# Performance work log

Measured on AMD Instinct MI355X. Metric: run time of the kernel, lower is better.

The kernel has to match this reference:

```python
import jax, jax.numpy as jnp
import numpy as np
from jax import lax

B, S = 2, 1024
T = B * S
HIDDEN, Q_LORA_RANK = 7168, 1536
N_HEADS, HEAD_DIM, ROPE_DIM = 64, 128, 64
INDEX_TOPK = 2048
QUANT_BLOCK = 128
F8_MAX = 448.0  # float8_e4m3fn max
SOFTMAX_SCALE = HEAD_DIM ** -0.5


def quant_dequant_ue8m0(x):
    """Simulate per-128-block fp8(e4m3) quantization with ue8m0 (power-of-2, ceil) scales."""
    shp = x.shape
    xb = x.reshape(shp[:-1] + (shp[-1] // QUANT_BLOCK, QUANT_BLOCK))
    amax = jnp.max(jnp.abs(xb), axis=-1, keepdims=True)
    scale = jnp.exp2(jnp.ceil(jnp.log2(jnp.maximum(amax, 1e-4) / F8_MAX)))
    q = jnp.clip(xb / scale, -F8_MAX, F8_MAX).astype(jnp.float8_e4m3fn).astype(jnp.float32)
    return (q * scale).reshape(shp)


def rope_cos_sin(positions):
    half = ROPE_DIM // 2
    inv_freq = 1.0 / (10000.0 ** (jnp.arange(half, dtype=jnp.float32) * 2.0 / ROPE_DIM))
    ang = positions.astype(jnp.float32)[:, None] * inv_freq[None, :]  # [T, half]
    return jnp.cos(ang), jnp.sin(ang)


def apply_rope(x, cos, sin):
    half = x.shape[-1] // 2
    x1, x2 = x[..., :half], x[..., half:]
    return jnp.concatenate([x1 * cos - x2 * sin, x1 * sin + x2 * cos], axis=-1)


def setup_inputs() -> dict:
    key = jax.random.key(0)
    k0, k1, k2, k3, k4 = jax.random.split(key, 5)
    std = 0.02
    hidden_states = jax.random.normal(k0, (T, HIDDEN), jnp.float32)
    q_lora = jax.random.normal(k1, (T, Q_LORA_RANK), jnp.float32)
    wq_b = jax.random.normal(k2, (N_HEADS * HEAD_DIM, Q_LORA_RANK), jnp.float32) * std
    wk = jax.random.normal(k3, (HEAD_DIM, HIDDEN), jnp.float32) * std
    k_norm_w = jnp.ones((HEAD_DIM,), jnp.float32)
    k_norm_b = jnp.zeros((HEAD_DIM,), jnp.float32)
    w_proj = jax.random.normal(k4, (N_HEADS, HIDDEN), jnp.float32) * std
    positions = jnp.tile(jnp.arange(S, dtype=jnp.int32), B)  # local position within each sequence
    seq_lens = jnp.full((B,), S, dtype=jnp.int32)
    return {"hidden_states": hidden_states, "q_lora": q_lora, "wq_b": wq_b, "wk": wk,
            "k_norm_w": k_norm_w, "k_norm_b": k_norm_b, "w_proj": w_proj,
            "positions": positions, "seq_lens": seq_lens}


def reference(hidden_states, q_lora, wq_b, wk, k_norm_w, k_norm_b, w_proj, positions, seq_lens):
    # --- projections ---
    q = (q_lora @ wq_b.T).reshape(T, N_HEADS, HEAD_DIM)
    k = hidden_states @ wk.T  # [T, HEAD_DIM]
    # k_norm: LayerNorm(head_dim, eps=1e-6) in fp32
    mu = jnp.mean(k, axis=-1, keepdims=True)
    kc = k - mu
    k = kc * lax.rsqrt(jnp.mean(kc * kc, axis=-1, keepdims=True) + 1e-6) * k_norm_w + k_norm_b
    # --- RoPE on first ROPE_DIM dims of q (per head) and k ---
    cos, sin = rope_cos_sin(positions)
    q = jnp.concatenate([apply_rope(q[..., :ROPE_DIM], cos[:, None, :], sin[:, None, :]),
                         q[..., ROPE_DIM:]], axis=-1)
    k = jnp.concatenate([apply_rope(k[..., :ROPE_DIM], cos, sin), k[..., ROPE_DIM:]], axis=-1)
    # --- fp8 ue8m0 quant-dequant (simulates q_fp8 / per_token_quant_and_transform) ---
    q = quant_dequant_ue8m0(q)
    k = quant_dequant_ue8m0(k)
    # --- head weights (weights_proj, head-count and softmax scaling folded in) ---
    weights = (hidden_states @ w_proj.T) * (N_HEADS ** -0.5) * SOFTMAX_SCALE  # [T, H]
    # --- variable-length causal bounds (compute_cu_seqlen_kv_bounds_nocache) ---
    cu = jnp.concatenate([jnp.zeros((1,), jnp.int32), jnp.cumsum(seq_lens).astype(jnp.int32)])
    batch_ids = jnp.repeat(jnp.arange(seq_lens.shape[0], dtype=jnp.int32), seq_lens,
                           total_repeat_length=T)
    ks_ = cu[batch_ids]                                   # start of each token's KV window
    local_pos = jnp.arange(T, dtype=jnp.int32) - ks_
    ke_ = ks_ + local_pos + 1                             # exclusive end (causal)
    pos_n = jnp.arange(T, dtype=jnp.int32)
    mask = (pos_n[None, :] >= ks_[:, None]) & (pos_n[None, :] < ke_[:, None])  # [T, T]
    # --- fp8_mqa_logits: logits[m,n] = sum_h w[m,h] * relu(q[m,h] . k[n]) ---
    qh = jnp.transpose(q, (1, 0, 2))  # [H, T, D]
    wh = weights.T                    # [H, T]
    def step(acc, hw):
        qh_i, w_i = hw
        return acc + jax.nn.relu(qh_i @ k.T) * w_i[:, None], None
    logits, _ = lax.scan(step, jnp.zeros((T, T), jnp.float32), (qh, wh))
    logits = jnp.where(mask, logits, -jnp.inf)
    # --- top-k selection + local-index remap ---
    k_take = min(INDEX_TOPK, T)
    _, idx = lax.top_k(logits, k_take)
    local = idx - ks_[:, None]
    valid = (local >= 0) & (idx < ke_[:, None])
    topk_indices = jnp.where(valid, local, -1).astype(jnp.int32)
    return logits, topk_indices
```

## Files before the change

kernel.cpp:

```cpp
#include <hip/hip_runtime.h>
#include <math.h>
#include <stdint.h>

#define T_TOK 2048
#define HIDDEN 7168
#define RANK 1536
#define NH 64
#define HD 128
#define NQ (NH*HD)
#define RH 32
#define KSPLIT 8
#define KCHUNK (HIDDEN/KSPLIT)
#define NKW 192

#define MASK_VAL (-3.0e38f)

typedef short bf16x8 __attribute__((ext_vector_type(8)));
typedef float f32x4  __attribute__((ext_vector_type(4)));

#define GLL16(src, dst) __builtin_amdgcn_global_load_lds( \
    (const __attribute__((address_space(1))) void*)(src), \
    (__attribute__((address_space(3))) void*)(dst), 16, 0, 0)

__device__ __forceinline__ float qd_e4m3(float x){
  float ax = fabsf(x);
  float s = (x < 0.f) ? -1.f : 1.f;
  float q;
  if (ax < 0.015625f) {
    q = rintf(ax * 512.f) * 0.001953125f;
  } else {
    int e; (void)frexpf(ax, &e);
    float quant = ldexpf(1.f, e - 4);
    q = rintf(ax / quant) * quant;
  }
  return s * q;
}

__device__ __forceinline__ float ue8m0_scale(float amax){
  float y = fmaxf(amax, 1e-4f) / 448.f;
  int e; float m = frexpf(y, &e);
  int ce = (m == 0.5f) ? (e - 1) : e;
  return ldexpf(1.f, ce);
}

__device__ __forceinline__ unsigned short f2bf_rne(float x){
  unsigned int u = __float_as_uint(x);
  unsigned int r = u + 0x7FFFu + ((u >> 16) & 1u);
  return (unsigned short)(r >> 16);
}

__device__ __forceinline__ void split_bf16(float x, unsigned short& hi, unsigned short& lo){
  unsigned int u = __float_as_uint(x);
  hi = (unsigned short)(u >> 16);
  float xh = __uint_as_float(u & 0xFFFF0000u);
  lo = f2bf_rne(x - xh);
}

__global__ void kt_cossin(const int* __restrict__ pos, float* __restrict__ cost,
                          float* __restrict__ sint){
  int idx = blockIdx.x*256 + threadIdx.x;
  if (idx >= T_TOK*RH) return;
  int t = idx >> 5, j = idx & 31;
  float ex = (float)(2*j) / 64.0f;
  float p10 = (float)pow(10000.0, (double)ex);
  float invf = 1.0f / p10;
  float ang = (float)pos[t] * invf;
  cost[idx] = (float)cos((double)ang);
  sint[idx] = (float)sin((double)ang);
}

__global__ __launch_bounds__(256) void kw_split(const float* __restrict__ Wk,
                                                const float* __restrict__ Wp,
                                                unsigned short* __restrict__ Bh,
                                                unsigned short* __restrict__ Bl){
  int idx = blockIdx.x*256 + threadIdx.x;
  int e0 = idx*8;
  if (e0 >= NKW*HIDDEN) return;
  int n = e0 / HIDDEN, k = e0 - n*HIDDEN;
  const float* src = (n < HD) ? (Wk + (size_t)n*HIDDEN + k) : (Wp + (size_t)(n-HD)*HIDDEN + k);
  float4 a0 = *(const float4*)src;
  float4 a1 = *(const float4*)(src+4);
  float f[8] = {a0.x,a0.y,a0.z,a0.w,a1.x,a1.y,a1.z,a1.w};
  unsigned short h[8], l[8];
  #pragma unroll
  for (int i=0;i<8;i++) split_bf16(f[i], h[i], l[i]);
  *(uint4*)(Bh + e0) = *(const uint4*)h;
  *(uint4*)(Bl + e0) = *(const uint4*)l;
}

__global__ __launch_bounds__(256,2) void kfat(const float* __restrict__ A,
                                              const float* __restrict__ B,
                                              const float* __restrict__ cost,
                                              const float* __restrict__ sint,
                                              unsigned short* __restrict__ q16,
                                              const float* __restrict__ H,
                                              const unsigned short* __restrict__ Bhg,
                                              const unsigned short* __restrict__ Blg,
                                              float* __restrict__ P){
  __shared__ char smem[33792] __attribute__((aligned(16)));
  int bid = blockIdx.x;
  int tid = threadIdx.x, lane = tid & 63;

  if (bid >= 256){
    int kb_id = bid - 256;
    unsigned short* Ah = (unsigned short*)smem;
    unsigned short* Al = Ah + 128*32;
    unsigned short* Bh = Al + 128*32;
    unsigned short* Bl = Bh + 128*32;
    float (*amx)[2] = (float(*)[2])(smem + 32768);
    int n0 = (kb_id & 63)*128, m0 = (kb_id >> 6)*128;
    int w = tid >> 6, wr = w >> 1, wc = w & 1;
    int row = tid >> 1, half = tid & 1;
    const float* Arow = A + (size_t)(m0+row)*RANK + half*16;
    const float* Brow = B + (size_t)(n0+row)*RANK + half*16;
    int sw = ((row >> 1) & 3) << 4;
    int wb0 = row*64 + half*32;
    f32x4 acc[4][4];
    #pragma unroll
    for (int i=0;i<4;i++)
      #pragma unroll
      for (int j=0;j<4;j++)
        #pragma unroll
        for (int r=0;r<4;r++) acc[i][j][r] = 0.f;

    for (int kb = 0; kb < RANK; kb += 32){
      float4 av4[4], bv4[4];
      #pragma unroll
      for (int c=0;c<4;c++) av4[c] = *(const float4*)(Arow + kb + 4*c);
      #pragma unroll
      for (int c=0;c<4;c++) bv4[c] = *(const float4*)(Brow + kb + 4*c);
      __syncthreads();
      {
        unsigned short h[16], l[16];
        const float* f = (const float*)av4;
        #pragma unroll
        for (int i=0;i<16;i++) split_bf16(f[i], h[i], l[i]);
        *(uint4*)((char*)Ah + ((wb0   )^sw)) = *(const uint4*)&h[0];
        *(uint4*)((char*)Ah + ((wb0+16)^sw)) = *(const uint4*)&h[8];
        *(uint4*)((char*)Al + ((wb0   )^sw)) = *(const uint4*)&l[0];
        *(uint4*)((char*)Al + ((wb0+16)^sw)) = *(const uint4*)&l[8];
        const float* g = (const float*)bv4;
        #pragma unroll
        for (int i=0;i<16;i++) split_bf16(g[i], h[i], l[i]);
        *(uint4*)((char*)Bh + ((wb0   )^sw)) = *(const uint4*)&h[0];
        *(uint4*)((char*)Bh + ((wb0+16)^sw)) = *(const uint4*)&h[8];
        *(uint4*)((char*)Bl + ((wb0   )^sw)) = *(const uint4*)&l[0];
        *(uint4*)((char*)Bl + ((wb0+16)^sw)) = *(const uint4*)&l[8];
      }
      __syncthreads();
      bf16x8 ah[4], bh[4], tmp[4];
      #pragma unroll
      for (int mf=0;mf<4;mf++){
        int rl = wr*64 + mf*16 + (lane&15);
        int ad = (rl*64 + ((lane>>4)*16)) ^ ((((rl>>1)&3))<<4);
        ah[mf] = *(const bf16x8*)((const char*)Ah + ad);
      }
      #pragma unroll
      for (int nf=0;nf<4;nf++){
        int rl = wc*64 + nf*16 + (lane&15);
        int ad = (rl*64 + ((lane>>4)*16)) ^ ((((rl>>1)&3))<<4);
        bh[nf] = *(const bf16x8*)((const char*)Bh + ad);
      }
      #pragma unroll
      for (int mf=0;mf<4;mf++)
        #pragma unroll
        for (int nf=0;nf<4;nf++)
          acc[mf][nf] = __builtin_amdgcn_mfma_f32_16x16x32_bf16(ah[mf], bh[nf], acc[mf][nf], 0,0,0);
      #pragma unroll
      for (int mf=0;mf<4;mf++){
        int rl = wr*64 + mf*16 + (lane&15);
        int ad = (rl*64 + ((lane>>4)*16)) ^ ((((rl>>1)&3))<<4);
        tmp[mf] = *(const bf16x8*)((const char*)Al + ad);
      }
      #pragma unroll
      for (int mf=0;mf<4;mf++)
        #pragma unroll
        for (int nf=0;nf<4;nf++)
          acc[mf][nf] = __builtin_amdgcn_mfma_f32_16x16x32_bf16(tmp[mf], bh[nf], acc[mf][nf], 0,0,0);
      #pragma unroll
      for (int nf=0;nf<4;nf++){
        int rl = wc*64 + nf*16 + (lane&15);
        int ad = (rl*64 + ((lane>>4)*16)) ^ ((((rl>>1)&3))<<4);
        tmp[nf] = *(const bf16x8*)((const char*)Bl + ad);
      }
      #pragma unroll
      for (int mf=0;mf<4;mf++)
        #pragma unroll
        for (int nf=0;nf<4;nf++)
          acc[mf][nf] = __builtin_amdgcn_mfma_f32_16x16x32_bf16(ah[mf], tmp[nf], acc[mf][nf], 0,0,0);
    }

    if (wc == 0){
      #pragma unroll
      for (int mf=0;mf<4;mf++)
        #pragma unroll
        for (int r=0;r<4;r++){
          int t = m0 + wr*64 + mf*16 + (lane>>4)*4 + r;
          #pragma unroll
          for (int nf=0;nf<2;nf++){
            int d0 = nf*16 + (lane&15);
            float c = cost[t*RH + d0], s = sint[t*RH + d0];
            float x1 = acc[mf][nf][r], x2 = acc[mf][nf+2][r];
            acc[mf][nf][r]   = __fsub_rn(__fmul_rn(x1,c), __fmul_rn(x2,s));
            acc[mf][nf+2][r] = __fadd_rn(__fmul_rn(x1,s), __fmul_rn(x2,c));
          }
        }
    }
    float pm[16];
    #pragma unroll
    for (int mf=0;mf<4;mf++)
      #pragma unroll
      for (int r=0;r<4;r++){
        float m1 = fmaxf(fabsf(acc[mf][0][r]), fabsf(acc[mf][1][r]));
        float m2 = fmaxf(fabsf(acc[mf][2][r]), fabsf(acc[mf][3][r]));
        pm[mf*4+r] = fmaxf(m1, m2);
      }
    #pragma unroll
    for (int msk=1; msk<16; msk<<=1)
      #pragma unroll
      for (int i=0;i<16;i++) pm[i] = fmaxf(pm[i], __shfl_xor(pm[i], msk, 16));
    if ((lane & 15) == 0){
      #pragma unroll
      for (int mf=0;mf<4;mf++)
        #pragma unroll
        for (int r=0;r<4;r++)
          amx[wr*64 + mf*16 + (lane>>4)*4 + r][wc] = pm[mf*4+r];
    }
    __syncthreads();
    #pragma unroll
    for (int mf=0;mf<4;mf++)
      #pragma unroll
      for (int r=0;r<4;r++){
        int rl = wr*64 + mf*16 + (lane>>4)*4 + r;
        int t = m0 + rl;
        float scl = ue8m0_scale(fmaxf(amx[rl][0], amx[rl][1]));
        #pragma unroll
        for (int nf=0;nf<4;nf++){
          float v = acc[mf][nf][r];
          float qv = qd_e4m3(v / scl) * scl;
          q16[(size_t)t*NQ + n0 + wc*64 + nf*16 + (lane&15)] = f2bf_rne(qv);
        }
      }
  } else {
    unsigned short* Ah = (unsigned short*)smem;
    unsigned short* Al = Ah + 64*32;
    unsigned short* Bh = Al + 64*32;
    unsigned short* Bl = Bh + NKW*32;
    int b2 = bid;
    int ks = b2 & 7, m0 = (b2 >> 3)*64, k0 = ks*KCHUNK;
    int w = tid >> 6, wr = w >> 1, wc = w & 1;
    int ar = tid >> 2, ac = (tid & 3)*8;
    const float* Arow = H + (size_t)(m0+ar)*HIDDEN + k0 + ac;
    int awb = (ar*64 + ac*2) ^ (((ar>>1)&3)<<4);
    f32x4 acc[2][6];
    #pragma unroll
    for (int i=0;i<2;i++)
      #pragma unroll
      for (int j=0;j<6;j++)
        #pragma unroll
        for (int r=0;r<4;r++) acc[i][j][r] = 0.f;

    for (int kb = 0; kb < KCHUNK; kb += 32){
      float4 a0 = *(const float4*)(Arow + kb);
      float4 a1 = *(const float4*)(Arow + kb + 4);
      __syncthreads();
      {
        float f[8] = {a0.x,a0.y,a0.z,a0.w,a1.x,a1.y,a1.z,a1.w};
        unsigned short h[8], l[8];
        #pragma unroll
        for (int i=0;i<8;i++) split_bf16(f[i], h[i], l[i]);
        *(uint4*)((char*)Ah + awb) = *(const uint4*)h;
        *(uint4*)((char*)Al + awb) = *(const uint4*)l;
      }
      #pragma unroll
      for (int i=0;i<3;i++){
        int ch = w + 4*i;
        int o = ch*1024 + lane*16;
        int row = o >> 6;
        int cb = (o & 63) ^ (((row>>1)&3)<<4);
        size_t srcoff = (size_t)row*HIDDEN + k0 + kb + (cb>>1);
        GLL16(Bhg + srcoff, (char*)Bh + ch*1024);
        GLL16(Blg + srcoff, (char*)Bl + ch*1024);
      }
      __syncthreads();
      bf16x8 ah[2], alr[2], bh[6], bl[6];
      #pragma unroll
      for (int mf=0;mf<2;mf++){
        int rl = wr*32 + mf*16 + (lane&15);
        int ad = (rl*64 + ((lane>>4)*16)) ^ (((rl>>1)&3)<<4);
        ah[mf]  = *(const bf16x8*)((const char*)Ah + ad);
        alr[mf] = *(const bf16x8*)((const char*)Al + ad);
      }
      #pragma unroll
      for (int nf=0;nf<6;nf++){
        int jl = wc*96 + nf*16 + (lane&15);
        int ad = (jl*64 + ((lane>>4)*16)) ^ (((jl>>1)&3)<<4);
        bh[nf] = *(const bf16x8*)((const char*)Bh + ad);
        bl[nf] = *(const bf16x8*)((const char*)Bl + ad);
      }
      #pragma unroll
      for (int mf=0;mf<2;mf++)
        #pragma unroll
        for (int nf=0;nf<6;nf++){
          acc[mf][nf] = __builtin_amdgcn_mfma_f32_16x16x32_bf16(ah[mf],  bh[nf], acc[mf][nf], 0,0,0);
          acc[mf][nf] = __builtin_amdgcn_mfma_f32_16x16x32_bf16(alr[mf], bh[nf], acc[mf][nf], 0,0,0);
          acc[mf][nf] = __builtin_amdgcn_mfma_f32_16x16x32_bf16(ah[mf],  bl[nf], acc[mf][nf], 0,0,0);
        }
    }
    #pragma unroll
    for (int mf=0;mf<2;mf++)
      #pragma unroll
      for (int r=0;r<4;r++){
        int t = m0 + wr*32 + mf*16 + (lane>>4)*4 + r;
        #pragma unroll
        for (int nf=0;nf<6;nf++){
          int n = wc*96 + nf*16 + (lane&15);
          P[((size_t)ks*T_TOK + t)*NKW + n] = acc[mf][nf][r];
        }
      }
  }
}

__global__ __launch_bounds__(128) void kc2(const float* __restrict__ P,
                                           const float* __restrict__ knw,
                                           const float* __restrict__ knb,
                                           const float* __restrict__ cost,
                                           const float* __restrict__ sint,
                                           unsigned short* __restrict__ k16,
                                           float* __restrict__ abuf){
  __shared__ float sh[128];
  __shared__ float red[128];
  int t = blockIdx.x, d = threadIdx.x;
  float v = 0.f;
  #pragma unroll
  for (int s=0;s<KSPLIT;s++) v += P[((size_t)s*T_TOK + t)*NKW + d];
  if (d < NH){
    float wv = 0.f;
    #pragma unroll
    for (int s=0;s<KSPLIT;s++) wv += P[((size_t)s*T_TOK + t)*NKW + HD + d];
    wv = wv * 0.125f;
    wv = wv * 0.08838834764831845f;
    abuf[(size_t)t*NH + d] = wv;
  }
  red[d] = v; __syncthreads();
  for (int s=64;s>0;s>>=1){ if (d<s) red[d] += red[d+s]; __syncthreads(); }
  float mu = red[0] * (1.0f/128.0f); __syncthreads();
  float kc = v - mu;
  red[d] = kc*kc; __syncthreads();
  for (int s=64;s>0;s>>=1){ if (d<s) red[d] += red[d+s]; __syncthreads(); }
  float var = red[0] * (1.0f/128.0f); __syncthreads();
  float rs = 1.0f / sqrtf(var + 1e-6f);
  float nv = ((kc * rs) * knw[d]) + knb[d];
  sh[d] = nv; __syncthreads();
  float rv;
  if (d < RH)            rv = sh[d]*cost[t*RH + d]      - sh[d+RH]*sint[t*RH + d];
  else if (d < 2*RH)     rv = sh[d-RH]*sint[t*RH + d-RH] + sh[d]*cost[t*RH + d-RH];
  else                   rv = nv;
  red[d] = fabsf(rv); __syncthreads();
  for (int s=64;s>0;s>>=1){ if (d<s) red[d] = fmaxf(red[d], red[d+s]); __syncthreads(); }
  float scale = ue8m0_scale(red[0]);
  k16[(size_t)t*HD + d] = f2bf_rne(qd_e4m3(rv / scale) * scale);
}

__global__ __launch_bounds__(256,2) void ke2(const unsigned short* __restrict__ q16,
                                             const unsigned short* __restrict__ k16,
                                             const float* __restrict__ W,
                                             const int* __restrict__ seq,
                                             float* __restrict__ out){
  __shared__ unsigned short Kt[128*128];
  __shared__ unsigned short Qt[2][64*128];
  __shared__ float Wl[64*64];
  int j0 = blockIdx.x*128, t0 = blockIdx.y*64;
  int tid = threadIdx.x;
  int s0 = seq[0];
  int ks0 = (t0 < s0) ? 0 : s0;
  if (j0 > t0 + 63 || j0 + 127 < ks0){
    int tl = tid >> 2, c0 = (tid & 3) * 32;
    float4 m4 = make_float4(MASK_VAL, MASK_VAL, MASK_VAL, MASK_VAL);
    float* rowp = out + (size_t)(t0+tl)*T_TOK + j0 + c0;
    #pragma unroll
    for (int c=0;c<32;c+=4) *(float4*)(rowp + c) = m4;
    return;
  }
  int lane = tid & 63, w = tid >> 6, wt = w >> 1, wj = w & 1;
  #pragma unroll
  for (int is=0; is<8; ++is){
    int o = is*4096 + w*1024 + lane*16;
    int row = o >> 8;
    int os = o ^ ((row & 7) << 4);
    int col = (os & 255) >> 1;
    GLL16(k16 + (size_t)(j0 + row)*HD + col, (char*)Kt + is*4096 + w*1024);
  }
  {
    int tl = tid >> 2, h0 = (tid & 3) * 16;
    float wv[16];
    #pragma unroll
    for (int c=0;c<4;c++) *(float4*)&wv[4*c] = *(const float4*)(W + (size_t)(t0+tl)*NH + h0 + 4*c);
    #pragma unroll
    for (int i=0;i<16;i++) Wl[(h0+i)*64 + tl] = wv[i];
  }
  #pragma unroll
  for (int is=0; is<4; ++is){
    int o = is*4096 + w*1024 + lane*16;
    int row = o >> 8;
    int os = o ^ ((row & 7) << 4);
    int col = (os & 255) >> 1;
    GLL16(q16 + (size_t)(t0 + row)*NQ + 0*HD + col, (char*)&Qt[0][0] + is*4096 + w*1024);
  }
  __syncthreads();
  bf16x8 bk[4][4];
  #pragma unroll
  for (int jf=0;jf<4;jf++){
    int jl = wj*64 + jf*16 + (lane&15);
    int sz = (jl & 7) << 4;
    #pragma unroll
    for (int kf=0;kf<4;kf++)
      bk[jf][kf] = *(const bf16x8*)((const char*)Kt + ((jl*256 + kf*64 + ((lane>>4)*16)) ^ sz));
  }
  bool skip = (j0 + wj*64 > t0 + wt*32 + 31) || (j0 + wj*64 + 63 < ks0);
  f32x4 acc[2][4];
  #pragma unroll
  for (int a=0;a<2;a++)
    #pragma unroll
    for (int b=0;b<4;b++)
      #pragma unroll
      for (int r=0;r<4;r++) acc[a][b][r] = 0.f;

  for (int h = 0; h < NH; ++h){
    if (h < NH-1){
      char* dst = (char*)&Qt[(h+1)&1][0];
      #pragma unroll
      for (int is=0; is<4; ++is){
        int o = is*4096 + w*1024 + lane*16;
        int row = o >> 8;
        int os = o ^ ((row & 7) << 4);
        int col = (os & 255) >> 1;
        GLL16(q16 + (size_t)(t0 + row)*NQ + (size_t)(h+1)*HD + col, dst + is*4096 + w*1024);
      }
    }
    if (!skip){
      const char* qb = (const char*)&Qt[h&1][0];
      bf16x8 aq[2][4];
      #pragma unroll
      for (int tf=0;tf<2;tf++){
        int tl = wt*32 + tf*16 + (lane&15);
        int sz = (tl & 7) << 4;
        #pragma unroll
        for (int kf=0;kf<4;kf++)
          aq[tf][kf] = *(const bf16x8*)(qb + ((tl*256 + kf*64 + ((lane>>4)*16)) ^ sz));
      }
      f32x4 pp[2][4];
      #pragma unroll
      for (int a=0;a<2;a++)
        #pragma unroll
        for (int b=0;b<4;b++)
          #pragma unroll
          for (int r=0;r<4;r++) pp[a][b][r] = 0.f;
      #pragma unroll
      for (int kf=0;kf<4;kf++)
        #pragma unroll
        for (int tf=0;tf<2;tf++)
          #pragma unroll
          for (int jf=0;jf<4;jf++)
            pp[tf][jf] = __builtin_amdgcn_mfma_f32_16x16x32_bf16(aq[tf][kf], bk[jf][kf], pp[tf][jf], 0,0,0);
      #pragma unroll
      for (int tf=0;tf<2;tf++)
        #pragma unroll
        for (int r=0;r<4;r++){
          float wv = Wl[h*64 + wt*32 + tf*16 + (lane>>4)*4 + r];
          #pragma unroll
          for (int jf=0;jf<4;jf++)
            acc[tf][jf][r] = fmaf(wv, fmaxf(pp[tf][jf][r], 0.f), acc[tf][jf][r]);
        }
    }
    __syncthreads();
  }
  #pragma unroll
  for (int tf=0;tf<2;tf++)
    #pragma unroll
    for (int r=0;r<4;r++){
      int t = t0 + wt*32 + tf*16 + (lane>>4)*4 + r;
      #pragma unroll
      for (int jf=0;jf<4;jf++){
        int j = j0 + wj*64 + jf*16 + (lane&15);
        bool ok = (j >= ks0) && (j <= t);
        out[(size_t)t*T_TOK + j] = ok ? acc[tf][jf][r] : MASK_VAL;
      }
    }
}

__global__ __launch_bounds__(256) void kf_topk(const float* __restrict__ logits,
                                               const int* __restrict__ seq,
                                               float* __restrict__ outIdx){
  __shared__ unsigned long long keys[1024];
  int t = blockIdx.x, tid = threadIdx.x;
  int s0 = seq[0];
  int ks = (t < s0) ? 0 : s0;
  int nv = t - ks + 1;
  for (int i = tid; i < 1024; i += 256){
    unsigned long long key = 0ull;
    if (i < nv){
      float v = logits[(size_t)t*T_TOK + ks + i];
      unsigned int b = __float_as_uint(v);
      unsigned int ov = (b & 0x80000000u) ? ~b : (b | 0x80000000u);
      key = ((unsigned long long)ov << 32) | (unsigned long long)(0x7FFFFFFFu - (unsigned)i);
    }
    keys[i] = key;
  }
  for (int size = 2; size <= 1024; size <<= 1){
    for (int stride = size >> 1; stride > 0; stride >>= 1){
      __syncthreads();
      for (int i = tid; i < 1024; i += 256){
        int p = i ^ stride;
        if (p > i){
          bool up = (i & size) == 0;
          unsigned long long a = keys[i], b2 = keys[p];
          if (up ? (a < b2) : (a > b2)){ keys[i] = b2; keys[p] = a; }
        }
      }
    }
  }
  __syncthreads();
  for (int p = tid; p < T_TOK; p += 256){
    float o = -1.0f;
    if (p < nv){
      unsigned int low = (unsigned int)(keys[p] & 0xFFFFFFFFull);
      o = (float)(int)(0x7FFFFFFFu - low);
    }
    outIdx[(size_t)t*T_TOK + p] = o;
  }
}

extern "C" void kernel_launch(void* const* d_in, const int* in_sizes, int n_in,
                              void* d_out, int out_size, void* d_ws, size_t ws_size,
                              hipStream_t stream){
  const float* hidden  = (const float*)d_in[0];
  const float* q_lora  = (const float*)d_in[1];
  const float* wq_b    = (const float*)d_in[2];
  const float* wk      = (const float*)d_in[3];
  const float* knw     = (const float*)d_in[4];
  const float* knb     = (const float*)d_in[5];
  const float* wproj   = (const float*)d_in[6];
  const int* positions = (const int*)d_in[7];
  const int* seq       = (const int*)d_in[8];

  char* ws = (char*)d_ws;
  unsigned short* q16 = (unsigned short*)ws;              ws += (size_t)T_TOK*NQ*2;
  float* P = (float*)ws;                                  ws += (size_t)KSPLIT*T_TOK*NKW*4;
  unsigned short* Whg = (unsigned short*)ws;              ws += (size_t)NKW*HIDDEN*2;
  unsigned short* Wlg = (unsigned short*)ws;              ws += (size_t)NKW*HIDDEN*2;
  unsigned short* k16 = (unsigned short*)ws;              ws += (size_t)T_TOK*HD*2;
  float* abuf = (float*)ws;                               ws += (size_t)T_TOK*NH*4;
  float* cost = (float*)ws;                               ws += (size_t)T_TOK*RH*4;
  float* sint = (float*)ws;                               ws += (size_t)T_TOK*RH*4;

  float* logits = (float*)d_out;
  float* topk   = logits + (size_t)T_TOK*T_TOK;

  kt_cossin<<<(T_TOK*RH)/256, 256, 0, stream>>>(positions, cost, sint);
  kw_split <<<(NKW*HIDDEN/8 + 255)/256, 256, 0, stream>>>(wk, wproj, Whg, Wlg);
  kfat     <<<1280, 256, 0, stream>>>(q_lora, wq_b, cost, sint, q16,
                                      hidden, Whg, Wlg, P);
  kc2      <<<T_TOK, 128, 0, stream>>>(P, knw, knb, cost, sint, k16, abuf);
  ke2      <<<dim3(T_TOK/128, T_TOK/64), 256, 0, stream>>>(q16, k16, abuf, seq, logits);
  kf_topk  <<<T_TOK, 256, 0, stream>>>(logits, seq, topk);
}
```

Before: 334.0 us.

## Rewrite top-k bitonic sort with register and wave-shuffle stages

The per-row bitonic sort in kf_topk now keeps four keys per thread in registers. Strides 1-2 compare within registers, strides 4-128 use cross-lane shuffles within a 64-wide wavefront, and only the strides of 256 and 512 go through LDS with barriers. This replaces dozens of LDS round-trips and __syncthreads per row with mostly barrier-free register and shuffle work. Keys are bit-inverted so an ascending sort gives descending order, and the logits load becomes vectorized float4. It adds macro complexity, and correctness depends on the wave64 shuffle layout.

```diff
diff --git a/kernel.cpp b/kernel.cpp
--- a/kernel.cpp
+++ b/kernel.cpp
@@ -489,46 +489,95 @@
     }
 }
 
+#define KF_REG(SIZE, S) { \
+  _Pragma("unroll") \
+  for (int e=0;e<4;e++){ int pe = e ^ (S); \
+    if (pe > e){ \
+      bool up = (((base + e) & (SIZE)) == 0); \
+      unsigned long long x = k[e], y = k[pe]; \
+      bool sw = up ? (x > y) : (x < y); \
+      if (sw){ k[e] = y; k[pe] = x; } } } }
+
+#define KF_SHFL(SIZE, S) { \
+  bool keepmin = (((base & (S)) == 0) == ((base & (SIZE)) == 0)); \
+  _Pragma("unroll") \
+  for (int e=0;e<4;e++){ \
+    unsigned long long o = __shfl_xor(k[e], (S)>>2, 64); \
+    unsigned long long mn = k[e] < o ? k[e] : o; \
+    unsigned long long mx = k[e] < o ? o : k[e]; \
+    k[e] = keepmin ? mn : mx; } }
+
+#define KF_LDS(SIZE, S) { \
+  __syncthreads(); \
+  _Pragma("unroll") \
+  for (int e=0;e<4;e++) lk[base+e] = k[e]; \
+  __syncthreads(); \
+  bool keepmin = (((base & (S)) == 0) == ((base & (SIZE)) == 0)); \
+  _Pragma("unroll") \
+  for (int e=0;e<4;e++){ \
+    unsigned long long o = lk[(base+e) ^ (S)]; \
+    unsigned long long mn = k[e] < o ? k[e] : o; \
+    unsigned long long mx = k[e] < o ? o : k[e]; \
+    k[e] = keepmin ? mn : mx; } }
+
 __global__ __launch_bounds__(256) void kf_topk(const float* __restrict__ logits,
                                                const int* __restrict__ seq,
                                                float* __restrict__ outIdx){
-  __shared__ unsigned long long keys[1024];
+  __shared__ unsigned long long lk[1024];
   int t = blockIdx.x, tid = threadIdx.x;
   int s0 = seq[0];
   int ks = (t < s0) ? 0 : s0;
   int nv = t - ks + 1;
-  for (int i = tid; i < 1024; i += 256){
-    unsigned long long key = 0ull;
-    if (i < nv){
-      float v = logits[(size_t)t*T_TOK + ks + i];
-      unsigned int b = __float_as_uint(v);
-      unsigned int ov = (b & 0x80000000u) ? ~b : (b | 0x80000000u);
-      key = ((unsigned long long)ov << 32) | (unsigned long long)(0x7FFFFFFFu - (unsigned)i);
-    }
-    keys[i] = key;
-  }
-  for (int size = 2; size <= 1024; size <<= 1){
-    for (int stride = size >> 1; stride > 0; stride >>= 1){
-      __syncthreads();
-      for (int i = tid; i < 1024; i += 256){
-        int p = i ^ stride;
-        if (p > i){
-          bool up = (i & size) == 0;
-          unsigned long long a = keys[i], b2 = keys[p];
-          if (up ? (a < b2) : (a > b2)){ keys[i] = b2; keys[p] = a; }
-        }
-      }
-    }
-  }
-  __syncthreads();
-  for (int p = tid; p < T_TOK; p += 256){
+  int base = tid * 4;
+  unsigned long long k[4];
+  {
+    float4 v4 = make_float4(0.f,0.f,0.f,0.f);
+    if (base + 3 < nv)      v4 = *(const float4*)(logits + (size_t)t*T_TOK + ks + base);
+    else {
+      float* vp = (float*)&v4;
+      #pragma unroll
+      for (int e=0;e<4;e++) if (base+e < nv) vp[e] = logits[(size_t)t*T_TOK + ks + base + e];
+    }
+    const float* vp = (const float*)&v4;
+    #pragma unroll
+    for (int e=0;e<4;e++){
+      int i = base + e;
+      unsigned long long key = 0ull;
+      if (i < nv){
+        unsigned int b = __float_as_uint(vp[e]);
+        unsigned int ov = (b & 0x80000000u) ? ~b : (b | 0x80000000u);
+        key = ((unsigned long long)ov << 32) | (unsigned long long)(0x7FFFFFFFu - (unsigned)i);
+      }
+      k[e] = ~key;
+    }
+  }
+  KF_REG(2,1);
+  KF_REG(4,2);   KF_REG(4,1);
+  KF_SHFL(8,4);  KF_REG(8,2);  KF_REG(8,1);
+  KF_SHFL(16,8); KF_SHFL(16,4); KF_REG(16,2); KF_REG(16,1);
+  KF_SHFL(32,16); KF_SHFL(32,8); KF_SHFL(32,4); KF_REG(32,2); KF_REG(32,1);
+  KF_SHFL(64,32); KF_SHFL(64,16); KF_SHFL(64,8); KF_SHFL(64,4); KF_REG(64,2); KF_REG(64,1);
+  KF_SHFL(128,64); KF_SHFL(128,32); KF_SHFL(128,16); KF_SHFL(128,8); KF_SHFL(128,4); KF_REG(128,2); KF_REG(128,1);
+  KF_SHFL(256,128); KF_SHFL(256,64); KF_SHFL(256,32); KF_SHFL(256,16); KF_SHFL(256,8); KF_SHFL(256,4); KF_REG(256,2); KF_REG(256,1);
+  KF_LDS(512,256);
+  KF_SHFL(512,128); KF_SHFL(512,64); KF_SHFL(512,32); KF_SHFL(512,16); KF_SHFL(512,8); KF_SHFL(512,4); KF_REG(512,2); KF_REG(512,1);
+  KF_LDS(1024,512);
+  KF_LDS(1024,256);
+  KF_SHFL(1024,128); KF_SHFL(1024,64); KF_SHFL(1024,32); KF_SHFL(1024,16); KF_SHFL(1024,8); KF_SHFL(1024,4); KF_REG(1024,2); KF_REG(1024,1);
+
+  #pragma unroll
+  for (int e=0;e<4;e++){
+    int p = base + e;
     float o = -1.0f;
     if (p < nv){
-      unsigned int low = (unsigned int)(keys[p] & 0xFFFFFFFFull);
+      unsigned long long key = ~k[e];
+      unsigned int low = (unsigned int)(key & 0xFFFFFFFFull);
       o = (float)(int)(0x7FFFFFFFu - low);
     }
     outIdx[(size_t)t*T_TOK + p] = o;
   }
+  for (int p = 1024 + tid; p < T_TOK; p += 256)
+    outIdx[(size_t)t*T_TOK + p] = -1.0f;
 }
 
 extern "C" void kernel_launch(void* const* d_in, const int* in_sizes, int n_in,
```

Result: faster. 302.6 us (-9.4%).
